# Optimization experiments

Hardware: AMD Instinct MI355X
Metric: run time of the kernel (lower is better)

The kernel has to match this reference:

```python
import jax, jax.numpy as jnp
import numpy as np
import math

B, N, D = 16, 2048, 256

def setup_inputs() -> dict:
    key = jax.random.key(0)
    kq, kk, kv = jax.random.split(key, 3)
    query = jax.random.normal(kq, (B, N, D), dtype=jnp.float32)
    k = jax.random.normal(kk, (B, N, D), dtype=jnp.float32)
    value = jax.random.normal(kv, (B, D, N), dtype=jnp.float32)  # channel-first [B, d_v, N]
    return {"query": query, "key": k, "value": value, "mask": 0}

def reference(query, key, value, mask):
    d_k = query.shape[-1]
    scale = 1.0 / math.sqrt(d_k)
    # scores: [B, N, N]
    scores = jnp.einsum('bnd,bmd->bnm', query, key) * scale
    p_attn = jax.nn.softmax(scores, axis=-1)
    # mask is a static Python int flag gating dropout; mask=0 -> no dropout (deterministic reference)
    if mask:
        pass  # dropout intentionally disabled in deterministic reference
    # out = p_attn @ value^T  -> [B, N, d_v]; module returns out.transpose(-2,-1) -> [B, d_v, N]
    out_t = jnp.einsum('bnm,bdm->bdn', p_attn, value)
    return (out_t, p_attn)
```

## Files before the change

kernel.cpp:

```cpp
#include <hip/hip_runtime.h>
#include <hip/hip_bf16.h>


using bf16x8 = __attribute__((ext_vector_type(8))) short;
using f32x4  = __attribute__((ext_vector_type(4))) float;

__device__ __forceinline__ short f2bf(float f) {
    unsigned u = __float_as_uint(f);
    u += 0x7fffu + ((u >> 16) & 1u);
    return (short)(u >> 16);
}
__device__ __forceinline__ f32x4 mfma16(bf16x8 a, bf16x8 b, f32x4 c) {
    return __builtin_amdgcn_mfma_f32_16x16x32_bf16(a, b, c, 0, 0, 0);
}

__device__ __forceinline__ void bar_lgkm() {
    asm volatile("s_waitcnt lgkmcnt(0)\n\ts_barrier" ::: "memory");
}
__device__ __forceinline__ void bar_vm4() {
    asm volatile("s_waitcnt vmcnt(4) lgkmcnt(0)\n\ts_barrier" ::: "memory");
}

#define AS1(p) ((const __attribute__((address_space(1))) void*)(p))
#define AS3(p) ((__attribute__((address_space(3))) void*)(p))

constexpr float LOG2E = 1.4426950408889634f;

__global__ __launch_bounds__(256)
void convert_qkv(const float* __restrict__ Q, const float* __restrict__ K,
                 const float* __restrict__ V, short* __restrict__ Qb,
                 short* __restrict__ Kb, short* __restrict__ Vb, size_t n8)
{
    size_t i = (size_t)blockIdx.x * 256 + threadIdx.x;
    const float* src;
    short* dst;
    float scale = 1.0f;
    if (i < n8)            { src = Q;  dst = Qb; scale = 0.0625f; }
    else if (i < 2 * n8)   { i -= n8;      src = K; dst = Kb; }
    else                   { i -= 2 * n8;  src = V; dst = Vb; }
    const f32x4* s4 = (const f32x4*)src;
    f32x4 a = __builtin_nontemporal_load(s4 + i * 2);
    f32x4 b = __builtin_nontemporal_load(s4 + i * 2 + 1);
    bf16x8 v;
    v[0] = f2bf(a[0] * scale); v[1] = f2bf(a[1] * scale);
    v[2] = f2bf(a[2] * scale); v[3] = f2bf(a[3] * scale);
    v[4] = f2bf(b[0] * scale); v[5] = f2bf(b[1] * scale);
    v[6] = f2bf(b[2] * scale); v[7] = f2bf(b[3] * scale);
    *(bf16x8*)(dst + i * 8) = v;
}

__global__ __launch_bounds__(512, 2)
void fused_attn(const short* __restrict__ Qb, const short* __restrict__ Kb,
                const short* __restrict__ Vb, float* __restrict__ Pout,
                float* __restrict__ outT)
{
    __shared__ __align__(16) short Klds[2][64 * 256];
    __shared__ __align__(16) short Vlds[2][256 * 64];
    __shared__ __align__(16) short Plds[128 * 64];
    float* lpart = (float*)Plds;

    const unsigned g  = blockIdx.x;
    const unsigned wg = (g & 7) * 32 + (g >> 3);
    const int b  = (int)(wg >> 4);
    const int nb = (int)(wg & 15);

    const int tid  = threadIdx.x;
    const int lane = tid & 63;
    const int wave = tid >> 6;
    const int wn  = wave >> 1;
    const int wm  = wave & 1;
    const int l15 = lane & 15;
    const int l4  = lane >> 4;

    const short* Kbase = Kb + (size_t)b * (2048 * 256);
    const short* Vbase = Vb + (size_t)b * (256 * 2048);

    const short* Qp = Qb + ((size_t)b * 2048 + (size_t)nb * 128) * 256;
    bf16x8 qf[2][8];
#pragma unroll
    for (int mf = 0; mf < 2; mf++)
#pragma unroll
        for (int ks = 0; ks < 8; ks++)
            qf[mf][ks] = *(const bf16x8*)(
                Qp + (size_t)(wn * 32 + mf * 16 + l15) * 256 + ks * 32 + l4 * 8);

    auto stage_k = [&](int t, int buf) {
#pragma unroll
        for (int i = 0; i < 4; i++) {
            int ml = i * 16 + wave * 2 + (lane >> 5);
            int c  = lane & 31;
            int cs = (c & 24) | ((c ^ ml) & 7);
            __builtin_amdgcn_global_load_lds(
                AS1(Kbase + (size_t)(t * 64 + ml) * 256 + cs * 8),
                AS3(&Klds[buf][i * 4096 + wave * 512]), 16, 0, 0);
        }
    };
    auto stage_v = [&](int t, int buf) {
#pragma unroll
        for (int i = 0; i < 4; i++) {
            int d  = i * 64 + wave * 8 + (lane >> 3);
            int c  = lane & 7;
            int cs = c ^ (d & 7);
            __builtin_amdgcn_global_load_lds(
                AS1(Vbase + (size_t)d * 2048 + t * 64 + cs * 8),
                AS3(&Vlds[buf][i * 4096 + wave * 512]), 16, 0, 0);
        }
    };
    auto stage_k128 = [&](int t, int which) {
#pragma unroll
        for (int i = 0; i < 8; i++) {
            int ml = i * 16 + wave * 2 + (lane >> 5);
            int c  = lane & 31;
            int cs = (c & 24) | ((c ^ ml) & 7);
            short* dst = which ? &Vlds[0][0] : &Klds[0][0];
            __builtin_amdgcn_global_load_lds(
                AS1(Kbase + (size_t)(t * 128 + ml) * 256 + cs * 8),
                AS3(dst + i * 4096 + wave * 512), 16, 0, 0);
        }
    };

    auto qkt = [&](int buf, f32x4 sacT[2][2]) {
        __builtin_amdgcn_s_setprio(1);
#pragma unroll
        for (int ks = 0; ks < 8; ks++) {
            bf16x8 kf[2];
#pragma unroll
            for (int nf = 0; nf < 2; nf++) {
                int m  = wm * 32 + nf * 16 + l15;
                int ch = (ks * 4 + l4) ^ (m & 7);
                kf[nf] = *(const bf16x8*)((const char*)&Klds[buf][0] + m * 512 + ch * 16);
            }
#pragma unroll
            for (int mf = 0; mf < 2; mf++)
#pragma unroll
                for (int nf = 0; nf < 2; nf++)
                    sacT[mf][nf] = mfma16(kf[nf], qf[mf][ks], sacT[mf][nf]);
        }
        __builtin_amdgcn_s_setprio(0);
    };
    auto qkt128 = [&](int which, f32x4 sacT[2][4]) {
        const char* kb = which ? (const char*)&Vlds[0][0] : (const char*)&Klds[0][0];
        __builtin_amdgcn_s_setprio(1);
#pragma unroll
        for (int ks = 0; ks < 8; ks++) {
            bf16x8 kf[4];
#pragma unroll
            for (int nf = 0; nf < 4; nf++) {
                int m  = wm * 64 + nf * 16 + l15;
                int ch = (ks * 4 + l4) ^ (m & 7);
                kf[nf] = *(const bf16x8*)(kb + m * 512 + ch * 16);
            }
#pragma unroll
            for (int mf = 0; mf < 2; mf++)
#pragma unroll
                for (int nf = 0; nf < 4; nf++)
                    sacT[mf][nf] = mfma16(kf[nf], qf[mf][ks], sacT[mf][nf]);
        }
        __builtin_amdgcn_s_setprio(0);
    };

    float lacc[2] = {0.f, 0.f};
    stage_k128(0, 0);
    for (int t = 0; t < 16; t++) {
        __syncthreads();
        if (t + 1 < 16) stage_k128(t + 1, (t + 1) & 1);
        f32x4 sacT[2][4];
#pragma unroll
        for (int mf = 0; mf < 2; mf++)
#pragma unroll
            for (int nf = 0; nf < 4; nf++)
                sacT[mf][nf] = f32x4{0.f, 0.f, 0.f, 0.f};
        qkt128(t & 1, sacT);
#pragma unroll
        for (int mf = 0; mf < 2; mf++)
#pragma unroll
            for (int nf = 0; nf < 4; nf++)
#pragma unroll
                for (int r = 0; r < 4; r++)
                    lacc[mf] += exp2f(sacT[mf][nf][r] * LOG2E);
    }
    stage_k(0, 0);
#pragma unroll
    for (int mf = 0; mf < 2; mf++) {
        lacc[mf] += __shfl_xor(lacc[mf], 16);
        lacc[mf] += __shfl_xor(lacc[mf], 32);
    }
    if (l4 == 0) {
        lpart[wave * 32 + 0 * 16 + l15] = lacc[0];
        lpart[wave * 32 + 1 * 16 + l15] = lacc[1];
    }
    __syncthreads();
    stage_v(0, 0);
    float rl[2];
#pragma unroll
    for (int mf = 0; mf < 2; mf++)
        rl[mf] = 1.0f / (lpart[(wn * 2 + 0) * 32 + mf * 16 + l15] +
                         lpart[(wn * 2 + 1) * 32 + mf * 16 + l15]);

    f32x4 oac[4][4];
#pragma unroll
    for (int i = 0; i < 4; i++)
#pragma unroll
        for (int j = 0; j < 4; j++)
            oac[i][j] = f32x4{0.f, 0.f, 0.f, 0.f};

    float* prow = Pout + ((size_t)b * 2048 + (size_t)nb * 128) * 2048;

    __syncthreads();

    for (int t = 0; t < 32; t++) {
        f32x4 sacT[2][2];
#pragma unroll
        for (int mf = 0; mf < 2; mf++)
#pragma unroll
            for (int nf = 0; nf < 2; nf++)
                sacT[mf][nf] = f32x4{0.f, 0.f, 0.f, 0.f};
        qkt(t & 1, sacT);

        if (t + 1 < 32) {
            stage_k(t + 1, (t + 1) & 1);
            stage_v(t + 1, (t + 1) & 1);
        }

        f32x4 pv4[2][2];
#pragma unroll
        for (int mf = 0; mf < 2; mf++)
#pragma unroll
            for (int nf = 0; nf < 2; nf++) {
#pragma unroll
                for (int r = 0; r < 4; r++)
                    pv4[mf][nf][r] = exp2f(sacT[mf][nf][r] * LOG2E) * rl[mf];
                short4 ps;
                ps.x = f2bf(pv4[mf][nf][0]); ps.y = f2bf(pv4[mf][nf][1]);
                ps.z = f2bf(pv4[mf][nf][2]); ps.w = f2bf(pv4[mf][nf][3]);
                const int n  = wn * 32 + mf * 16 + l15;
                const int mb = wm * 32 + nf * 16 + l4 * 4;
                const int ch = (mb >> 3) ^ (n & 7);
                *(short4*)((char*)Plds + n * 128 + ch * 16 + (mb & 7) * 2) = ps;
            }
        bar_lgkm();

#pragma unroll
        for (int mf = 0; mf < 2; mf++)
#pragma unroll
            for (int nf = 0; nf < 2; nf++) {
                const int n  = wn * 32 + mf * 16 + l15;
                const int m  = t * 64 + wm * 32 + nf * 16 + l4 * 4;
                __builtin_nontemporal_store(pv4[mf][nf],
                    (f32x4*)(prow + (size_t)n * 2048 + m));
            }

        const char* vb_ = (const char*)&Vlds[t & 1][0];
        __builtin_amdgcn_s_setprio(1);
#pragma unroll
        for (int ksl = 0; ksl < 2; ksl++) {
            bf16x8 vf[4], pf[4];
#pragma unroll
            for (int mf4 = 0; mf4 < 4; mf4++) {
                const int d  = wn * 64 + mf4 * 16 + l15;
                const int ch = (ksl * 4 + l4) ^ (d & 7);
                vf[mf4] = *(const bf16x8*)(vb_ + d * 128 + ch * 16);
            }
#pragma unroll
            for (int nf4 = 0; nf4 < 4; nf4++) {
                const int n  = wm * 64 + nf4 * 16 + l15;
                const int ch = (ksl * 4 + l4) ^ (n & 7);
                pf[nf4] = *(const bf16x8*)((const char*)Plds + n * 128 + ch * 16);
            }
#pragma unroll
            for (int mf4 = 0; mf4 < 4; mf4++)
#pragma unroll
                for (int nf4 = 0; nf4 < 4; nf4++)
                    oac[mf4][nf4] = mfma16(vf[mf4], pf[nf4], oac[mf4][nf4]);
        }
        __builtin_amdgcn_s_setprio(0);

        bar_vm4();
    }

    float* op = outT + (size_t)b * (256 * 2048) + (size_t)nb * 128;
#pragma unroll
    for (int mf4 = 0; mf4 < 4; mf4++)
#pragma unroll
        for (int nf4 = 0; nf4 < 4; nf4++)
#pragma unroll
            for (int r = 0; r < 4; r++) {
                int d = wn * 64 + mf4 * 16 + l4 * 4 + r;
                int n = wm * 64 + nf4 * 16 + l15;
                op[(size_t)d * 2048 + n] = oac[mf4][nf4][r];
            }
}

template<int BM, int BN, int BK>
__global__ __launch_bounds__(256)
void gemm_abt(const float* __restrict__ A, const float* __restrict__ B,
              float* __restrict__ C, int M, int N, int K,
              long strideA, long strideB, long strideC, float scale)
{
    const int b  = blockIdx.z;
    const int bm = blockIdx.y;
    const int bn = blockIdx.x;
    A += (size_t)b * strideA;
    B += (size_t)b * strideB;
    C += (size_t)b * strideC;

    constexpr int LDT = BK + 8;
    __shared__ __align__(16) short Alds[BM][LDT];
    __shared__ __align__(16) short Blds[BN][LDT];

    const int tid  = threadIdx.x;
    const int lane = tid & 63;
    const int wave = tid >> 6;
    const int wr   = wave >> 1;
    const int wc   = wave & 1;

    f32x4 acc[4][4];
#pragma unroll
    for (int m = 0; m < 4; m++)
#pragma unroll
        for (int n = 0; n < 4; n++)
            acc[m][n] = f32x4{0.f, 0.f, 0.f, 0.f};

    const float* Ab = A + (size_t)(bm * BM) * K;
    const float* Bb = B + (size_t)(bn * BN) * K;

    const int tr  = tid >> 4;
    const int tc4 = (tid & 15) << 2;

    for (int k0 = 0; k0 < K; k0 += BK) {
        __syncthreads();
#pragma unroll
        for (int r = tr; r < BM; r += 16) {
            const float4 v = *(const float4*)(Ab + (size_t)r * K + k0 + tc4);
            short4 s;
            s.x = f2bf(v.x); s.y = f2bf(v.y); s.z = f2bf(v.z); s.w = f2bf(v.w);
            *(short4*)&Alds[r][tc4] = s;
        }
#pragma unroll
        for (int r = tr; r < BN; r += 16) {
            const float4 v = *(const float4*)(Bb + (size_t)r * K + k0 + tc4);
            short4 s;
            s.x = f2bf(v.x); s.y = f2bf(v.y); s.z = f2bf(v.z); s.w = f2bf(v.w);
            *(short4*)&Blds[r][tc4] = s;
        }
        __syncthreads();

#pragma unroll
        for (int kk = 0; kk < BK; kk += 32) {
            const int ko = kk + ((lane >> 4) << 3);
            bf16x8 af[4], bfr[4];
#pragma unroll
            for (int m = 0; m < 4; m++)
                af[m] = *(const bf16x8*)&Alds[wr * 64 + m * 16 + (lane & 15)][ko];
#pragma unroll
            for (int n = 0; n < 4; n++)
                bfr[n] = *(const bf16x8*)&Blds[wc * 64 + n * 16 + (lane & 15)][ko];
#pragma unroll
            for (int m = 0; m < 4; m++)
#pragma unroll
                for (int n = 0; n < 4; n++)
                    acc[m][n] = __builtin_amdgcn_mfma_f32_16x16x32_bf16(
                        af[m], bfr[n], acc[m][n], 0, 0, 0);
        }
    }

    float* Cb = C + (size_t)(bm * BM) * N + (size_t)bn * BN;
    const int rbase = wr * 64 + ((lane >> 4) << 2);
    const int cbase = wc * 64 + (lane & 15);
#pragma unroll
    for (int m = 0; m < 4; m++)
#pragma unroll
        for (int n = 0; n < 4; n++)
#pragma unroll
            for (int r = 0; r < 4; r++)
                Cb[(size_t)(rbase + m * 16 + r) * N + cbase + n * 16] =
                    acc[m][n][r] * scale;
}

__global__ __launch_bounds__(256)
void softmax_rows(float* __restrict__ P)
{
    const size_t row = blockIdx.x;
    float* p = P + row * 2048;
    const int tid  = threadIdx.x;
    const int lane = tid & 63;
    const int wave = tid >> 6;

    float4 v0 = ((const float4*)p)[tid];
    float4 v1 = ((const float4*)p)[tid + 256];

    float m = fmaxf(fmaxf(fmaxf(v0.x, v0.y), fmaxf(v0.z, v0.w)),
                    fmaxf(fmaxf(v1.x, v1.y), fmaxf(v1.z, v1.w)));
#pragma unroll
    for (int off = 32; off; off >>= 1) m = fmaxf(m, __shfl_xor(m, off));

    __shared__ float sred[4];
    __shared__ float ssum[4];
    if (lane == 0) sred[wave] = m;
    __syncthreads();
    m = fmaxf(fmaxf(sred[0], sred[1]), fmaxf(sred[2], sred[3]));

    v0.x = expf(v0.x - m); v0.y = expf(v0.y - m);
    v0.z = expf(v0.z - m); v0.w = expf(v0.w - m);
    v1.x = expf(v1.x - m); v1.y = expf(v1.y - m);
    v1.z = expf(v1.z - m); v1.w = expf(v1.w - m);

    float s = (v0.x + v0.y + v0.z + v0.w) + (v1.x + v1.y + v1.z + v1.w);
#pragma unroll
    for (int off = 32; off; off >>= 1) s += __shfl_xor(s, off);
    if (lane == 0) ssum[wave] = s;
    __syncthreads();
    s = ssum[0] + ssum[1] + ssum[2] + ssum[3];

    const float r = 1.0f / s;
    v0.x *= r; v0.y *= r; v0.z *= r; v0.w *= r;
    v1.x *= r; v1.y *= r; v1.z *= r; v1.w *= r;

    ((float4*)p)[tid]       = v0;
    ((float4*)p)[tid + 256] = v1;
}

extern "C" void kernel_launch(void* const* d_in, const int* in_sizes, int n_in,
                              void* d_out, int out_size, void* d_ws, size_t ws_size,
                              hipStream_t stream)
{
    const float* Q  = (const float*)d_in[0];
    const float* Kk = (const float*)d_in[1];
    const float* V  = (const float*)d_in[2];

    float* outT = (float*)d_out;
    float* P    = outT + (size_t)16 * 256 * 2048;

    const size_t nQ = (size_t)16 * 2048 * 256;
    const long sQK = (long)2048 * 256;
    const long sP  = (long)2048 * 2048;
    const long sO  = (long)256 * 2048;

    const size_t needQKV = 3 * nQ * sizeof(short);

    if (ws_size >= needQKV) {
        short* Qb = (short*)d_ws;
        short* Kb = Qb + nQ;
        short* Vb = Kb + nQ;

        convert_qkv<<<dim3((unsigned)(3 * nQ / 8 / 256)), 256, 0, stream>>>(
            Q, Kk, V, Qb, Kb, Vb, nQ / 8);

        fused_attn<<<dim3(256), 512, 0, stream>>>(Qb, Kb, Vb, P, outT);
    } else {
        gemm_abt<128, 128, 64><<<dim3(16, 16, 16), 256, 0, stream>>>(
            Q, Kk, P, 2048, 2048, 256, sQK, sQK, sP, 0.0625f);
        softmax_rows<<<dim3(16 * 2048), 256, 0, stream>>>(P);
        gemm_abt<128, 128, 64><<<dim3(16, 2, 16), 256, 0, stream>>>(
            V, P, outT, 256, 2048, 2048, sO, sP, sO, 1.0f);
    }
}
```

Before: 162.7 us.

## Remap QK^T wave tiling to 64 query rows per wave and move P stores before barrier

Changes the wave-to-tile mapping for the QK^T phases so each wave holds 64 query rows of Q fragments and covers 16 key columns, instead of a 32x32 split. Each wave now loads one K fragment per k-step instead of two, which cuts LDS reads of K, but Q register usage doubles (32 bf16x8 vectors). Row-sum partials are now combined across four waves. The global nontemporal stores of P are issued before the LDS barrier rather than after, so they can overlap with it. The higher register pressure may lower occupancy or cause spills.

Result: slower. 207.2 us (+27.4%).

```diff
diff --git a/kernel.cpp b/kernel.cpp
--- a/kernel.cpp
+++ b/kernel.cpp
@@ -69,6 +69,8 @@
     const int wave = tid >> 6;
     const int wn  = wave >> 1;
     const int wm  = wave & 1;
+    const int wq  = wave >> 2;
+    const int wms = wave & 3;
     const int l15 = lane & 15;
     const int l4  = lane >> 4;
 
@@ -76,13 +78,13 @@
     const short* Vbase = Vb + (size_t)b * (256 * 2048);
 
     const short* Qp = Qb + ((size_t)b * 2048 + (size_t)nb * 128) * 256;
-    bf16x8 qf[2][8];
-#pragma unroll
-    for (int mf = 0; mf < 2; mf++)
+    bf16x8 qf[4][8];
+#pragma unroll
+    for (int mf = 0; mf < 4; mf++)
 #pragma unroll
         for (int ks = 0; ks < 8; ks++)
             qf[mf][ks] = *(const bf16x8*)(
-                Qp + (size_t)(wn * 32 + mf * 16 + l15) * 256 + ks * 32 + l4 * 8);
+                Qp + (size_t)(wq * 64 + mf * 16 + l15) * 256 + ks * 32 + l4 * 8);
 
     auto stage_k = [&](int t, int buf) {
 #pragma unroll
@@ -119,83 +121,81 @@
         }
     };
 
-    auto qkt = [&](int buf, f32x4 sacT[2][2]) {
+    auto qkt = [&](int buf, f32x4 sacT[4]) {
+        __builtin_amdgcn_s_setprio(1);
+#pragma unroll
+        for (int ks = 0; ks < 8; ks++) {
+            const int m  = wms * 16 + l15;
+            const int ch = (ks * 4 + l4) ^ (m & 7);
+            bf16x8 kf = *(const bf16x8*)((const char*)&Klds[buf][0] + m * 512 + ch * 16);
+#pragma unroll
+            for (int mf = 0; mf < 4; mf++)
+                sacT[mf] = mfma16(kf, qf[mf][ks], sacT[mf]);
+        }
+        __builtin_amdgcn_s_setprio(0);
+    };
+    auto qkt128 = [&](int which, f32x4 sacT[4][2]) {
+        const char* kb = which ? (const char*)&Vlds[0][0] : (const char*)&Klds[0][0];
         __builtin_amdgcn_s_setprio(1);
 #pragma unroll
         for (int ks = 0; ks < 8; ks++) {
             bf16x8 kf[2];
 #pragma unroll
             for (int nf = 0; nf < 2; nf++) {
-                int m  = wm * 32 + nf * 16 + l15;
-                int ch = (ks * 4 + l4) ^ (m & 7);
-                kf[nf] = *(const bf16x8*)((const char*)&Klds[buf][0] + m * 512 + ch * 16);
-            }
-#pragma unroll
-            for (int mf = 0; mf < 2; mf++)
-#pragma unroll
-                for (int nf = 0; nf < 2; nf++)
-                    sacT[mf][nf] = mfma16(kf[nf], qf[mf][ks], sacT[mf][nf]);
-        }
-        __builtin_amdgcn_s_setprio(0);
-    };
-    auto qkt128 = [&](int which, f32x4 sacT[2][4]) {
-        const char* kb = which ? (const char*)&Vlds[0][0] : (const char*)&Klds[0][0];
-        __builtin_amdgcn_s_setprio(1);
-#pragma unroll
-        for (int ks = 0; ks < 8; ks++) {
-            bf16x8 kf[4];
-#pragma unroll
-            for (int nf = 0; nf < 4; nf++) {
-                int m  = wm * 64 + nf * 16 + l15;
+                int m  = nf * 64 + wms * 16 + l15;
                 int ch = (ks * 4 + l4) ^ (m & 7);
                 kf[nf] = *(const bf16x8*)(kb + m * 512 + ch * 16);
             }
 #pragma unroll
-            for (int mf = 0; mf < 2; mf++)
-#pragma unroll
-                for (int nf = 0; nf < 4; nf++)
+            for (int mf = 0; mf < 4; mf++)
+#pragma unroll
+                for (int nf = 0; nf < 2; nf++)
                     sacT[mf][nf] = mfma16(kf[nf], qf[mf][ks], sacT[mf][nf]);
         }
         __builtin_amdgcn_s_setprio(0);
     };
 
-    float lacc[2] = {0.f, 0.f};
+    float lacc[4] = {0.f, 0.f, 0.f, 0.f};
     stage_k128(0, 0);
     for (int t = 0; t < 16; t++) {
         __syncthreads();
         if (t + 1 < 16) stage_k128(t + 1, (t + 1) & 1);
-        f32x4 sacT[2][4];
-#pragma unroll
-        for (int mf = 0; mf < 2; mf++)
-#pragma unroll
-            for (int nf = 0; nf < 4; nf++)
+        f32x4 sacT[4][2];
+#pragma unroll
+        for (int mf = 0; mf < 4; mf++)
+#pragma unroll
+            for (int nf = 0; nf < 2; nf++)
                 sacT[mf][nf] = f32x4{0.f, 0.f, 0.f, 0.f};
         qkt128(t & 1, sacT);
 #pragma unroll
-        for (int mf = 0; mf < 2; mf++)
-#pragma unroll
-            for (int nf = 0; nf < 4; nf++)
+        for (int mf = 0; mf < 4; mf++)
+#pragma unroll
+            for (int nf = 0; nf < 2; nf++)
 #pragma unroll
                 for (int r = 0; r < 4; r++)
                     lacc[mf] += exp2f(sacT[mf][nf][r] * LOG2E);
     }
     stage_k(0, 0);
 #pragma unroll
-    for (int mf = 0; mf < 2; mf++) {
+    for (int mf = 0; mf < 4; mf++) {
         lacc[mf] += __shfl_xor(lacc[mf], 16);
         lacc[mf] += __shfl_xor(lacc[mf], 32);
     }
-    if (l4 == 0) {
-        lpart[wave * 32 + 0 * 16 + l15] = lacc[0];
-        lpart[wave * 32 + 1 * 16 + l15] = lacc[1];
-    }
+    if (l4 == 0)
+#pragma unroll
+        for (int mf = 0; mf < 4; mf++)
+            lpart[wave * 64 + mf * 16 + l15] = lacc[mf];
     __syncthreads();
     stage_v(0, 0);
-    float rl[2];
-#pragma unroll
-    for (int mf = 0; mf < 2; mf++)
-        rl[mf] = 1.0f / (lpart[(wn * 2 + 0) * 32 + mf * 16 + l15] +
-                         lpart[(wn * 2 + 1) * 32 + mf * 16 + l15]);
+    float rl[4];
+#pragma unroll
+    for (int mf = 0; mf < 4; mf++) {
+        float s = 0.f;
+#pragma unroll
+        for (int j = 0; j < 4; j++)
+            s += lpart[(wq * 4 + j) * 64 + mf * 16 + l15];
+        rl[mf] = 1.0f / s;
+    }
 
     f32x4 oac[4][4];
 #pragma unroll
@@ -209,12 +209,10 @@
     __syncthreads();
 
     for (int t = 0; t < 32; t++) {
-        f32x4 sacT[2][2];
-#pragma unroll
-        for (int mf = 0; mf < 2; mf++)
-#pragma unroll
-            for (int nf = 0; nf < 2; nf++)
-                sacT[mf][nf] = f32x4{0.f, 0.f, 0.f, 0.f};
+        f32x4 sacT[4];
+#pragma unroll
+        for (int mf = 0; mf < 4; mf++)
+            sacT[mf] = f32x4{0.f, 0.f, 0.f, 0.f};
         qkt(t & 1, sacT);
 
         if (t + 1 < 32) {
@@ -222,33 +220,32 @@
             stage_v(t + 1, (t + 1) & 1);
         }
 
-        f32x4 pv4[2][2];
-#pragma unroll
-        for (int mf = 0; mf < 2; mf++)
-#pragma unroll
-            for (int nf = 0; nf < 2; nf++) {
-#pragma unroll
-                for (int r = 0; r < 4; r++)
-                    pv4[mf][nf][r] = exp2f(sacT[mf][nf][r] * LOG2E) * rl[mf];
-                short4 ps;
-                ps.x = f2bf(pv4[mf][nf][0]); ps.y = f2bf(pv4[mf][nf][1]);
-                ps.z = f2bf(pv4[mf][nf][2]); ps.w = f2bf(pv4[mf][nf][3]);
-                const int n  = wn * 32 + mf * 16 + l15;
-                const int mb = wm * 32 + nf * 16 + l4 * 4;
-                const int ch = (mb >> 3) ^ (n & 7);
-                *(short4*)((char*)Plds + n * 128 + ch * 16 + (mb & 7) * 2) = ps;
-            }
+        f32x4 pv4[4];
+#pragma unroll
+        for (int mf = 0; mf < 4; mf++)
+#pragma unroll
+            for (int r = 0; r < 4; r++)
+                pv4[mf][r] = exp2f(sacT[mf][r] * LOG2E) * rl[mf];
+
+#pragma unroll
+        for (int mf = 0; mf < 4; mf++) {
+            const int n = wq * 64 + mf * 16 + l15;
+            const int m = t * 64 + wms * 16 + l4 * 4;
+            __builtin_nontemporal_store(pv4[mf],
+                (f32x4*)(prow + (size_t)n * 2048 + m));
+        }
+
+#pragma unroll
+        for (int mf = 0; mf < 4; mf++) {
+            short4 ps;
+            ps.x = f2bf(pv4[mf][0]); ps.y = f2bf(pv4[mf][1]);
+            ps.z = f2bf(pv4[mf][2]); ps.w = f2bf(pv4[mf][3]);
+            const int n  = wq * 64 + mf * 16 + l15;
+            const int mb = wms * 16 + l4 * 4;
+            const int ch = (mb >> 3) ^ (n & 7);
+            *(short4*)((char*)Plds + n * 128 + ch * 16 + (mb & 7) * 2) = ps;
+        }
         bar_lgkm();
-
-#pragma unroll
-        for (int mf = 0; mf < 2; mf++)
-#pragma unroll
-            for (int nf = 0; nf < 2; nf++) {
-                const int n  = wn * 32 + mf * 16 + l15;
-                const int m  = t * 64 + wm * 32 + nf * 16 + l4 * 4;
-                __builtin_nontemporal_store(pv4[mf][nf],
-                    (f32x4*)(prow + (size_t)n * 2048 + m));
-            }
 
         const char* vb_ = (const char*)&Vlds[t & 1][0];
         __builtin_amdgcn_s_setprio(1);
```
